# Optimization experiments

Measured on AMD Instinct MI355X. Metric: run time of the kernel, lower is better.

The kernel has to match this reference:

```python
import jax, jax.numpy as jnp
import numpy as np

B, SQ, SKV, D, H = 4, 2048, 2048, 1024, 16
DH = D // H  # 64


def setup_inputs() -> dict:
    key = jax.random.key(0)
    ks = jax.random.split(key, 8)
    s = 0.02  # realistic init scale for weights
    return {
        "query": jax.random.normal(ks[0], (B, SQ, D), dtype=jnp.float32),
        "value": jax.random.normal(ks[1], (B, SKV, D), dtype=jnp.float32),
        "wq": jax.random.normal(ks[2], (H, D, DH), dtype=jnp.float32) * s,
        "bq": jnp.zeros((H, DH), dtype=jnp.float32),
        "wk": jax.random.normal(ks[3], (H, D, DH), dtype=jnp.float32) * s,
        "bk": jnp.zeros((H, DH), dtype=jnp.float32),
        "wv": jax.random.normal(ks[4], (H, D, DH), dtype=jnp.float32) * s,
        "bv": jnp.zeros((H, DH), dtype=jnp.float32),
        "wo": jax.random.normal(ks[5], (D, D), dtype=jnp.float32) * s,
        "bo": jnp.zeros((D,), dtype=jnp.float32),
    }


def reference(query, value, wq, bq, wk, bk, wv, bv, wo, bo):
    # Batched equivalent of the per-head Dense loop: [B,S,D] x [H,D,DH] -> [B,H,S,DH]
    q = jnp.einsum("bsd,hde->bhse", query, wq) + bq[None, :, None, :]
    k = jnp.einsum("bsd,hde->bhse", value, wk) + bk[None, :, None, :]
    v = jnp.einsum("bsd,hde->bhse", value, wv) + bv[None, :, None, :]
    scale = 1.0 / jnp.sqrt(jnp.asarray(DH, dtype=q.dtype))
    scores = jnp.einsum("bhqe,bhke->bhqk", q, k) * scale  # [B,H,SQ,SKV]
    align = jax.nn.softmax(scores, axis=-1)
    heads = jnp.einsum("bhqk,bhke->bhqe", align, v)  # [B,H,SQ,DH]
    # concat heads along feature dim (head order preserved)
    heads = jnp.transpose(heads, (0, 2, 1, 3)).reshape(B, SQ, D)
    return heads @ wo + bo
```

## Files before the change

### kernel.cpp

```cpp
#include <hip/hip_runtime.h>
#include <stdint.h>

#define DEVI __device__ __forceinline__

typedef __bf16  bf16x8 __attribute__((ext_vector_type(8)));
typedef float   f32x4  __attribute__((ext_vector_type(4)));
typedef float   f32x16 __attribute__((ext_vector_type(16)));
typedef uint32_t u32x4 __attribute__((ext_vector_type(4)));
typedef uint32_t u32x2v __attribute__((ext_vector_type(2)));
typedef uint16_t u16x8 __attribute__((ext_vector_type(8)));
typedef uint16_t u16x4 __attribute__((ext_vector_type(4)));

static constexpr int BB = 4, SQL = 2048, SKVL = 2048, DMODEL = 1024, NH = 16;
static constexpr int MROWS = BB * SQL;
static constexpr int KD = DMODEL;

DEVI uint16_t f2bf(float x) {
  uint32_t u = __builtin_bit_cast(uint32_t, x);
  u += 0x7FFFu + ((u >> 16) & 1u);
  return (uint16_t)(u >> 16);
}
DEVI uint32_t cvt2bf(float a, float b) {
  __bf16 x = (__bf16)a, y = (__bf16)b;
  return (uint32_t)__builtin_bit_cast(uint16_t, x) |
         ((uint32_t)__builtin_bit_cast(uint16_t, y) << 16);
}
DEVI f32x4 mfma16(bf16x8 a, bf16x8 b, f32x4 c) {
  return __builtin_amdgcn_mfma_f32_16x16x32_bf16(a, b, c, 0, 0, 0);
}
DEVI f32x16 mfma32(bf16x8 a, bf16x8 b, f32x16 c) {
  return __builtin_amdgcn_mfma_f32_32x32x16_bf16(a, b, c, 0, 0, 0);
}
DEVI void gload16(const void* g, void* l) {
  __builtin_amdgcn_global_load_lds((__attribute__((address_space(1))) const void*)g,
                                   (__attribute__((address_space(3))) void*)l, 16, 0, 0);
}
DEVI bf16x8 ldread(const void* p) { return __builtin_bit_cast(bf16x8, *(const u32x4*)p); }
DEVI u32x2v plswap(uint32_t a, uint32_t b) {
  return __builtin_amdgcn_permlane32_swap(a, b, false, false);
}

__global__ __launch_bounds__(256) void k_cvt(const float* __restrict__ q, const float* __restrict__ v,
                                             const float* __restrict__ wq, const float* __restrict__ wk,
                                             const float* __restrict__ wv, const float* __restrict__ wo,
                                             uint16_t* __restrict__ aq, uint16_t* __restrict__ av,
                                             uint16_t* __restrict__ wt) {
  const int bx = blockIdx.x;
  if (bx < 16384) {
    const int idx = bx * 256 + threadIdx.x;
    const int z = idx >> 20, f = idx & 1048575;
    const int n = f >> 10, d = f & 1023;
    const float* w = (z == 0) ? wq : (z == 1) ? wk : (z == 2) ? wv : wo;
    const float x = (z < 3) ? w[((n >> 6) << 16) + d * 64 + (n & 63)] : w[d * 1024 + n];
    wt[(size_t)z * 1048576 + f] = f2bf(x);
  } else {
    const int64_t n4 = (int64_t)MROWS * DMODEL / 4;
    for (int64_t i = (int64_t)(bx - 16384) * 256 + threadIdx.x; i < 2 * n4; i += (int64_t)2048 * 256) {
      const bool second = (i >= n4);
      const int64_t j = second ? i - n4 : i;
      const float4 x = (second ? (const float4*)v : (const float4*)q)[j];
      u16x4 o = { f2bf(x.x), f2bf(x.y), f2bf(x.z), f2bf(x.w) };
      *(u16x4*)((second ? av : aq) + j * 4) = o;
    }
  }
}

template <int MODE>
__global__ __launch_bounds__(256) void k_gemm(const uint16_t* __restrict__ A, const uint16_t* __restrict__ Bt,
                                              const float* __restrict__ bias, const float* __restrict__ biasB,
                                              void* __restrict__ outp, void* __restrict__ outpB,
                                              float oscale) {
  __shared__ __align__(16) uint16_t Al[2][128 * 64];
  __shared__ __align__(16) uint16_t Bl[2][128 * 64];
  const int tid = threadIdx.x;
  const int w = tid >> 6, ln = tid & 63;
  const int g = ln >> 4, lc = ln & 15;
  const int m0 = blockIdx.x * 128, n0 = blockIdx.y * 128;
  const int wm = (w >> 1) * 64, wn = (w & 1) * 64;
  const int srow = w * 32 + (ln >> 3);
  const int colp = (ln & 7) * 16;

  f32x4 acc[4][4] = {};

  auto stage = [&](int kt, int bs) {
    #pragma unroll
    for (int i = 0; i < 4; ++i) {
      const int row = srow + i * 8;
      const int colb = colp ^ ((row & 7) << 4);
      gload16((const char*)(A + (size_t)(m0 + row) * KD + kt * 64) + colb,
              (char*)&Al[bs][0] + w * 4096 + i * 1024);
      gload16((const char*)(Bt + (size_t)(n0 + row) * KD + kt * 64) + colb,
              (char*)&Bl[bs][0] + w * 4096 + i * 1024);
    }
  };

  stage(0, 0);
  asm volatile("s_waitcnt vmcnt(0)" ::: "memory");
  __builtin_amdgcn_s_barrier();
  __builtin_amdgcn_sched_barrier(0);

  int cur = 0;
  #pragma unroll 2
  for (int kt = 0; kt < KD / 64; ++kt) {
    if (kt + 1 < KD / 64) stage(kt + 1, cur ^ 1);
    const char* Ac = (const char*)&Al[cur][0];
    const char* Bc = (const char*)&Bl[cur][0];
    #pragma unroll
    for (int kk = 0; kk < 2; ++kk) {
      bf16x8 af[4], bfr[4];
      #pragma unroll
      for (int mt = 0; mt < 4; ++mt) {
        const int row = wm + mt * 16 + lc;
        af[mt] = ldread(Ac + row * 128 + ((kk * 64 + g * 16) ^ ((row & 7) << 4)));
      }
      #pragma unroll
      for (int nt = 0; nt < 4; ++nt) {
        const int row = wn + nt * 16 + lc;
        bfr[nt] = ldread(Bc + row * 128 + ((kk * 64 + g * 16) ^ ((row & 7) << 4)));
      }
      #pragma unroll
      for (int mt = 0; mt < 4; ++mt)
        #pragma unroll
        for (int nt = 0; nt < 4; ++nt)
          acc[mt][nt] = mfma16(af[mt], bfr[nt], acc[mt][nt]);
    }
    asm volatile("s_waitcnt vmcnt(0)" ::: "memory");
    __builtin_amdgcn_s_barrier();
    __builtin_amdgcn_sched_barrier(0);
    cur ^= 1;
  }

  #pragma unroll
  for (int nt = 0; nt < 4; ++nt) {
    const int n = n0 + wn + nt * 16 + lc;
    const int z = (MODE == 2) ? (n >> 10) : 0;
    const int nn = (MODE == 2) ? (n & 1023) : n;
    const float bv = (MODE == 2) ? (z ? biasB : bias)[nn] : bias[n];
    uint16_t* dst16 = (uint16_t*)((MODE == 2 && z) ? outpB : outp);
    #pragma unroll
    for (int mt = 0; mt < 4; ++mt) {
      #pragma unroll
      for (int r = 0; r < 4; ++r) {
        const int m = m0 + wm + mt * 16 + g * 4 + r;
        if (MODE != 1) {
          float val = acc[mt][nt][r] + bv;
          if (MODE == 0) val *= oscale;
          const int b = m >> 11, s = m & 2047, h = nn >> 6, e = nn & 63;
          dst16[((size_t)((b * NH + h) * SQL + s)) * 64 + e] = f2bf(val);
        } else {
          ((float*)outp)[(size_t)m * DMODEL + n] = acc[mt][nt][r] + bv;
        }
      }
    }
  }
}

__global__ __launch_bounds__(256, 3) void k_attn(const uint16_t* __restrict__ Qb,
                                                 const uint16_t* __restrict__ Kb,
                                                 const uint16_t* __restrict__ Vb,
                                                 uint16_t* __restrict__ Hd) {
  __shared__ __align__(16) uint16_t Kl[2][64 * 64];
  __shared__ __align__(16) uint16_t Vl[2][64 * 64];
  const int tid = threadIdx.x;
  const int w = tid >> 6, ln = tid & 63;
  const int ql = ln & 31, hi = ln >> 5;
  const int bsw = blockIdx.x;
  const int l = (bsw & 7) * 128 + (bsw >> 3);
  const int qx = l & 15, bh = l >> 4;
  const int q0 = qx * 128 + w * 32;

  const uint16_t* Qp = Qb + ((size_t)bh * SQL + q0 + ql) * 64;
  bf16x8 qf[4];
  #pragma unroll
  for (int s = 0; s < 4; ++s)
    qf[s] = __builtin_bit_cast(bf16x8, *(const u16x8*)(Qp + s * 16 + hi * 8));

  const uint16_t* Kbase = Kb + (size_t)bh * SKVL * 64;
  const uint16_t* Vbase = Vb + (size_t)bh * SKVL * 64;

  const int swl = (ln & 7) << 4;
  const int e0off = (hi << 4) ^ swl;
  const int rb = ql * 128;

  const int krow0 = w * 16 + (ln >> 3);
  const int kcolb = (((ln & 7) ^ (ln >> 3)) << 4);
  const int vkv = (tid & 31) * 2, ve0 = (tid >> 5) * 8;

  f32x16 acc0 = {}, acc1 = {};
  float lsum = 0.f;

  {
    #pragma unroll
    for (int i = 0; i < 2; ++i) {
      const int row = krow0 + i * 8;
      gload16((const char*)(Kbase + (size_t)row * 64) + kcolb,
              (char*)&Kl[0][0] + w * 2048 + i * 1024);
    }
    const u16x8 a = *(const u16x8*)(Vbase + (size_t)vkv * 64 + ve0);
    const u16x8 b = *(const u16x8*)(Vbase + (size_t)(vkv + 1) * 64 + ve0);
    #pragma unroll
    for (int i = 0; i < 8; ++i) {
      const int e = ve0 + i;
      *(uint32_t*)((char*)&Vl[0][0] + e * 128 + ((vkv * 2) ^ ((e & 7) << 4))) =
          (uint32_t)a[i] | ((uint32_t)b[i] << 16);
    }
  }
  __syncthreads();

  int cur = 0;
  for (int t = 0; t < SKVL / 64; ++t) {
    const bool pre = (t + 1 < SKVL / 64);
    u16x8 nv0, nv1;
    if (pre) {
      const uint16_t* Kc = Kbase + (size_t)(t + 1) * 4096;
      #pragma unroll
      for (int i = 0; i < 2; ++i) {
        const int row = krow0 + i * 8;
        gload16((const char*)(Kc + (size_t)row * 64) + kcolb,
                (char*)&Kl[cur ^ 1][0] + w * 2048 + i * 1024);
      }
      const uint16_t* Vc = Vbase + (size_t)(t + 1) * 4096;
      nv0 = *(const u16x8*)(Vc + (size_t)vkv * 64 + ve0);
      nv1 = *(const u16x8*)(Vc + (size_t)(vkv + 1) * 64 + ve0);
    }
    const char* Kc0 = (const char*)&Kl[cur][0];
    f32x16 s0 = {}, s1 = {};
    __builtin_amdgcn_s_setprio(1);
    #pragma unroll
    for (int s = 0; s < 4; ++s) {
      const int off = e0off ^ (s << 5);
      const bf16x8 k0 = ldread(Kc0 + rb + off);
      const bf16x8 k1 = ldread(Kc0 + 4096 + rb + off);
      s0 = mfma32(k0, qf[s], s0);
      s1 = mfma32(k1, qf[s], s1);
    }
    __builtin_amdgcn_s_setprio(0);
    float ps = 0.f;
    #pragma unroll
    for (int r = 0; r < 16; ++r) {
      s0[r] = __builtin_amdgcn_exp2f(s0[r]);
      s1[r] = __builtin_amdgcn_exp2f(s1[r]);
      ps += s0[r] + s1[r];
    }
    lsum += ps;
    uint32_t w32[2][4][2];
    #pragma unroll
    for (int c8 = 0; c8 < 4; ++c8) {
      #pragma unroll
      for (int p = 0; p < 2; ++p) {
        w32[0][c8][p] = cvt2bf(s0[4 * c8 + 2 * p], s0[4 * c8 + 2 * p + 1]);
        w32[1][c8][p] = cvt2bf(s1[4 * c8 + 2 * p], s1[4 * c8 + 2 * p + 1]);
      }
    }
    const char* Vc0 = (const char*)&Vl[cur][0];
    __builtin_amdgcn_s_setprio(1);
    #pragma unroll
    for (int u = 0; u < 4; ++u) {
      const int tt = u >> 1, ul = u & 1;
      const u32x2v e0 = plswap(w32[tt][2 * ul][0], w32[tt][2 * ul + 1][0]);
      const u32x2v e1 = plswap(w32[tt][2 * ul][1], w32[tt][2 * ul + 1][1]);
      u32x4 pj;
      pj[0] = e0[0]; pj[1] = e1[0]; pj[2] = e0[1]; pj[3] = e1[1];
      const bf16x8 pb = __builtin_bit_cast(bf16x8, pj);
      const int off = e0off ^ (u << 5);
      const bf16x8 v0 = ldread(Vc0 + rb + off);
      const bf16x8 v1 = ldread(Vc0 + 4096 + rb + off);
      acc0 = mfma32(v0, pb, acc0);
      acc1 = mfma32(v1, pb, acc1);
    }
    __builtin_amdgcn_s_setprio(0);
    if (pre) {
      #pragma unroll
      for (int i = 0; i < 8; ++i) {
        const int e = ve0 + i;
        *(uint32_t*)((char*)&Vl[cur ^ 1][0] + e * 128 + ((vkv * 2) ^ ((e & 7) << 4))) =
            (uint32_t)nv0[i] | ((uint32_t)nv1[i] << 16);
      }
    }
    __syncthreads();
    cur ^= 1;
  }
  {
    const float lt = lsum + __shfl_xor(lsum, 32);
    const float inv = __builtin_amdgcn_rcpf(lt);
    const int b = bh >> 4, h = bh & 15;
    uint16_t* op = Hd + ((size_t)(b * SQL + q0 + ql)) * DMODEL + h * 64;
    #pragma unroll
    for (int et = 0; et < 2; ++et) {
      #pragma unroll
      for (int r2 = 0; r2 < 8; ++r2) {
        const float v0 = (et ? acc1[2 * r2] : acc0[2 * r2]) * inv;
        const float v1 = (et ? acc1[2 * r2 + 1] : acc0[2 * r2 + 1]) * inv;
        const int e = et * 32 + 4 * hi + (r2 & 1) * 2 + (r2 >> 1) * 8;
        *(uint32_t*)(op + e) = cvt2bf(v0, v1);
      }
    }
  }
}

extern "C" void kernel_launch(void* const* d_in, const int* in_sizes, int n_in,
                              void* d_out, int out_size, void* d_ws, size_t ws_size,
                              hipStream_t stream) {
  const float* query = (const float*)d_in[0];
  const float* value = (const float*)d_in[1];
  const float* wq = (const float*)d_in[2];
  const float* bq = (const float*)d_in[3];
  const float* wk = (const float*)d_in[4];
  const float* bk = (const float*)d_in[5];
  const float* wv = (const float*)d_in[6];
  const float* bv = (const float*)d_in[7];
  const float* wo = (const float*)d_in[8];
  const float* bo = (const float*)d_in[9];

  const size_t SZ_ACT = (size_t)MROWS * DMODEL * 2;
  const size_t SZ_W   = (size_t)4 * DMODEL * DMODEL * 2;
  if (ws_size < 6 * SZ_ACT + SZ_W) return;

  char* ws = (char*)d_ws;
  uint16_t* Aq = (uint16_t*)ws;  ws += SZ_ACT;
  uint16_t* Av = (uint16_t*)ws;  ws += SZ_ACT;
  uint16_t* Wt = (uint16_t*)ws;  ws += SZ_W;
  uint16_t* Qb = (uint16_t*)ws;  ws += SZ_ACT;
  uint16_t* Kb = (uint16_t*)ws;  ws += SZ_ACT;
  uint16_t* Vb = (uint16_t*)ws;  ws += SZ_ACT;
  uint16_t* Hd = (uint16_t*)ws;  ws += SZ_ACT;

  const float QSCALE = 0.18033688011112042f;

  k_cvt<<<dim3(18432), dim3(256), 0, stream>>>(query, value, wq, wk, wv, wo, Aq, Av, Wt);
  k_gemm<0><<<dim3(64, 8), dim3(256), 0, stream>>>(Aq, Wt, bq, nullptr, Qb, nullptr, QSCALE);
  k_gemm<2><<<dim3(64, 16), dim3(256), 0, stream>>>(Av, Wt + 1048576, bk, bv, Kb, Vb, 1.0f);
  k_attn<<<dim3(1024), dim3(256), 0, stream>>>(Qb, Kb, Vb, Hd);
  k_gemm<1><<<dim3(64, 8), dim3(256), 0, stream>>>(Hd, Wt + 3145728, bo, nullptr, d_out, nullptr, 1.0f);
}
```

Baseline: 229.7 us.

## Tile weight transpose through LDS and merge Q/K/V projections into one launch

The weight conversion kernel now transposes 64x64 tiles through shared memory, giving coalesced float4 reads and 16-byte bf16 writes in place of one strided scalar element per thread. Grid size falls from 16384 weight blocks to 1024. The Q and K/V projection GEMMs are merged into one kernel with a 24-row grid that picks its input, weights, bias and output per segment, which removes a launch and lets all projection tiles run concurrently. The output GEMM becomes its own specialised kernel, and the removed template branching may slightly change register use.

```diff
diff --git a/kernel.cpp b/kernel.cpp
--- a/kernel.cpp
+++ b/kernel.cpp
@@ -46,16 +46,45 @@
                                              uint16_t* __restrict__ aq, uint16_t* __restrict__ av,
                                              uint16_t* __restrict__ wt) {
   const int bx = blockIdx.x;
-  if (bx < 16384) {
-    const int idx = bx * 256 + threadIdx.x;
-    const int z = idx >> 20, f = idx & 1048575;
-    const int n = f >> 10, d = f & 1023;
-    const float* w = (z == 0) ? wq : (z == 1) ? wk : (z == 2) ? wv : wo;
-    const float x = (z < 3) ? w[((n >> 6) << 16) + d * 64 + (n & 63)] : w[d * 1024 + n];
-    wt[(size_t)z * 1048576 + f] = f2bf(x);
+  const int tid = threadIdx.x;
+  if (bx < 1024) {
+    __shared__ float lds[64 * 65];
+    const float* src; int rstride; size_t obase; int d0;
+    if (bx < 768) {
+      const int zz = bx >> 8, rem = bx & 255, h = rem >> 4, dt = rem & 15;
+      d0 = dt * 64;
+      src = ((zz == 0) ? wq : (zz == 1) ? wk : wv) + (size_t)h * 65536;
+      rstride = 64;
+      obase = (size_t)zz * 1048576 + (size_t)h * 64 * 1024;
+    } else {
+      const int idx = bx - 768, dt = idx >> 4, nt = idx & 15;
+      d0 = dt * 64;
+      src = wo + nt * 64;
+      rstride = 1024;
+      obase = (size_t)3 * 1048576 + (size_t)(nt * 64) * 1024;
+    }
+    const int e4 = (tid & 15) * 4, dl0 = tid >> 4;
+    #pragma unroll
+    for (int p = 0; p < 4; ++p) {
+      const int dl = dl0 + p * 16;
+      const float4 x = *(const float4*)(src + (size_t)(d0 + dl) * rstride + e4);
+      float* row = &lds[dl * 65 + e4];
+      row[0] = x.x; row[1] = x.y; row[2] = x.z; row[3] = x.w;
+    }
+    __syncthreads();
+    const int er = tid >> 2, dp = tid & 3;
+    uint16_t tmp[16];
+    #pragma unroll
+    for (int i = 0; i < 16; ++i) tmp[i] = f2bf(lds[(dp * 16 + i) * 65 + er]);
+    uint16_t* orow = wt + obase + (size_t)er * 1024 + d0 + dp * 16;
+    u16x8 o0, o1;
+    #pragma unroll
+    for (int j = 0; j < 8; ++j) { o0[j] = tmp[j]; o1[j] = tmp[8 + j]; }
+    *(u16x8*)orow = o0;
+    *(u16x8*)(orow + 8) = o1;
   } else {
     const int64_t n4 = (int64_t)MROWS * DMODEL / 4;
-    for (int64_t i = (int64_t)(bx - 16384) * 256 + threadIdx.x; i < 2 * n4; i += (int64_t)2048 * 256) {
+    for (int64_t i = (int64_t)(bx - 1024) * 256 + tid; i < 2 * n4; i += (int64_t)2048 * 256) {
       const bool second = (i >= n4);
       const int64_t j = second ? i - n4 : i;
       const float4 x = (second ? (const float4*)v : (const float4*)q)[j];
@@ -65,11 +94,97 @@
   }
 }
 
-template <int MODE>
-__global__ __launch_bounds__(256) void k_gemm(const uint16_t* __restrict__ A, const uint16_t* __restrict__ Bt,
-                                              const float* __restrict__ bias, const float* __restrict__ biasB,
-                                              void* __restrict__ outp, void* __restrict__ outpB,
-                                              float oscale) {
+__global__ __launch_bounds__(256) void k_gemm3(const uint16_t* __restrict__ Aq, const uint16_t* __restrict__ Av,
+                                               const uint16_t* __restrict__ Wt,
+                                               const float* __restrict__ bq, const float* __restrict__ bk,
+                                               const float* __restrict__ bv,
+                                               uint16_t* __restrict__ Qb, uint16_t* __restrict__ Kb,
+                                               uint16_t* __restrict__ Vb, float qscale) {
+  __shared__ __align__(16) uint16_t Al[2][128 * 64];
+  __shared__ __align__(16) uint16_t Bl[2][128 * 64];
+  const int tid = threadIdx.x;
+  const int w = tid >> 6, ln = tid & 63;
+  const int g = ln >> 4, lc = ln & 15;
+  const int seg = blockIdx.y >> 3;
+  const int m0 = blockIdx.x * 128, n0 = (blockIdx.y & 7) * 128;
+  const uint16_t* A = (seg == 0) ? Aq : Av;
+  const uint16_t* Bt = Wt + (size_t)seg * 1048576;
+  const float* bias = (seg == 0) ? bq : (seg == 1) ? bk : bv;
+  uint16_t* outp = (seg == 0) ? Qb : (seg == 1) ? Kb : Vb;
+  const float oscale = (seg == 0) ? qscale : 1.0f;
+  const int wm = (w >> 1) * 64, wn = (w & 1) * 64;
+  const int srow = w * 32 + (ln >> 3);
+  const int colp = (ln & 7) * 16;
+
+  f32x4 acc[4][4] = {};
+
+  auto stage = [&](int kt, int bs) {
+    #pragma unroll
+    for (int i = 0; i < 4; ++i) {
+      const int row = srow + i * 8;
+      const int colb = colp ^ ((row & 7) << 4);
+      gload16((const char*)(A + (size_t)(m0 + row) * KD + kt * 64) + colb,
+              (char*)&Al[bs][0] + w * 4096 + i * 1024);
+      gload16((const char*)(Bt + (size_t)(n0 + row) * KD + kt * 64) + colb,
+              (char*)&Bl[bs][0] + w * 4096 + i * 1024);
+    }
+  };
+
+  stage(0, 0);
+  asm volatile("s_waitcnt vmcnt(0)" ::: "memory");
+  __builtin_amdgcn_s_barrier();
+  __builtin_amdgcn_sched_barrier(0);
+
+  int cur = 0;
+  #pragma unroll 2
+  for (int kt = 0; kt < KD / 64; ++kt) {
+    if (kt + 1 < KD / 64) stage(kt + 1, cur ^ 1);
+    const char* Ac = (const char*)&Al[cur][0];
+    const char* Bc = (const char*)&Bl[cur][0];
+    #pragma unroll
+    for (int kk = 0; kk < 2; ++kk) {
+      bf16x8 af[4], bfr[4];
+      #pragma unroll
+      for (int mt = 0; mt < 4; ++mt) {
+        const int row = wm + mt * 16 + lc;
+        af[mt] = ldread(Ac + row * 128 + ((kk * 64 + g * 16) ^ ((row & 7) << 4)));
+      }
+      #pragma unroll
+      for (int nt = 0; nt < 4; ++nt) {
+        const int row = wn + nt * 16 + lc;
+        bfr[nt] = ldread(Bc + row * 128 + ((kk * 64 + g * 16) ^ ((row & 7) << 4)));
+      }
+      #pragma unroll
+      for (int mt = 0; mt < 4; ++mt)
+        #pragma unroll
+        for (int nt = 0; nt < 4; ++nt)
+          acc[mt][nt] = mfma16(af[mt], bfr[nt], acc[mt][nt]);
+    }
+    asm volatile("s_waitcnt vmcnt(0)" ::: "memory");
+    __builtin_amdgcn_s_barrier();
+    __builtin_amdgcn_sched_barrier(0);
+    cur ^= 1;
+  }
+
+  #pragma unroll
+  for (int nt = 0; nt < 4; ++nt) {
+    const int n = n0 + wn + nt * 16 + lc;
+    const float bv_ = bias[n];
+    #pragma unroll
+    for (int mt = 0; mt < 4; ++mt) {
+      #pragma unroll
+      for (int r = 0; r < 4; ++r) {
+        const int m = m0 + wm + mt * 16 + g * 4 + r;
+        const float val = (acc[mt][nt][r] + bv_) * oscale;
+        const int b = m >> 11, s = m & 2047, h = n >> 6, e = n & 63;
+        outp[((size_t)((b * NH + h) * SQL + s)) * 64 + e] = f2bf(val);
+      }
+    }
+  }
+}
+
+__global__ __launch_bounds__(256) void k_gemmO(const uint16_t* __restrict__ A, const uint16_t* __restrict__ Bt,
+                                               const float* __restrict__ bias, float* __restrict__ outp) {
   __shared__ __align__(16) uint16_t Al[2][128 * 64];
   __shared__ __align__(16) uint16_t Bl[2][128 * 64];
   const int tid = threadIdx.x;
@@ -133,23 +248,13 @@
   #pragma unroll
   for (int nt = 0; nt < 4; ++nt) {
     const int n = n0 + wn + nt * 16 + lc;
-    const int z = (MODE == 2) ? (n >> 10) : 0;
-    const int nn = (MODE == 2) ? (n & 1023) : n;
-    const float bv = (MODE == 2) ? (z ? biasB : bias)[nn] : bias[n];
-    uint16_t* dst16 = (uint16_t*)((MODE == 2 && z) ? outpB : outp);
+    const float bv_ = bias[n];
     #pragma unroll
     for (int mt = 0; mt < 4; ++mt) {
       #pragma unroll
       for (int r = 0; r < 4; ++r) {
         const int m = m0 + wm + mt * 16 + g * 4 + r;
-        if (MODE != 1) {
-          float val = acc[mt][nt][r] + bv;
-          if (MODE == 0) val *= oscale;
-          const int b = m >> 11, s = m & 2047, h = nn >> 6, e = nn & 63;
-          dst16[((size_t)((b * NH + h) * SQL + s)) * 64 + e] = f2bf(val);
-        } else {
-          ((float*)outp)[(size_t)m * DMODEL + n] = acc[mt][nt][r] + bv;
-        }
+        outp[(size_t)m * DMODEL + n] = acc[mt][nt][r] + bv_;
       }
     }
   }
@@ -327,9 +432,8 @@
 
   const float QSCALE = 0.18033688011112042f;
 
-  k_cvt<<<dim3(18432), dim3(256), 0, stream>>>(query, value, wq, wk, wv, wo, Aq, Av, Wt);
-  k_gemm<0><<<dim3(64, 8), dim3(256), 0, stream>>>(Aq, Wt, bq, nullptr, Qb, nullptr, QSCALE);
-  k_gemm<2><<<dim3(64, 16), dim3(256), 0, stream>>>(Av, Wt + 1048576, bk, bv, Kb, Vb, 1.0f);
+  k_cvt<<<dim3(3072), dim3(256), 0, stream>>>(query, value, wq, wk, wv, wo, Aq, Av, Wt);
+  k_gemm3<<<dim3(64, 24), dim3(256), 0, stream>>>(Aq, Av, Wt, bq, bk, bv, Qb, Kb, Vb, QSCALE);
   k_attn<<<dim3(1024), dim3(256), 0, stream>>>(Qb, Kb, Vb, Hd);
-  k_gemm<1><<<dim3(64, 8), dim3(256), 0, stream>>>(Hd, Wt + 3145728, bo, nullptr, d_out, nullptr, 1.0f);
-}
+  k_gemmO<<<dim3(64, 8), dim3(256), 0, stream>>>(Hd, Wt + 3145728, bo, (float*)d_out);
+}
```

Result: faster. 216.7 us (-5.7%).
